# Optimization experiments

Hardware: AMD Instinct MI355X
Metric: run time of the kernel (lower is better)

Reference implementation:

```python
import jax, jax.numpy as jnp
import numpy as np

B, N, DIN, DOUT = 8, 2048, 512, 512

def setup_inputs() -> dict:
    key = jax.random.key(0)
    kx, ka, kw, kb, kattn = jax.random.split(key, 5)
    x = jax.random.normal(kx, (B, N, DIN), dtype=jnp.float32)
    adjacency_matrix = jax.random.randint(ka, (B, N, N), 0, 2, dtype=jnp.int32)
    # nn.Linear(in,out): weight [out,in], bias [out]
    lim_w = float(np.sqrt(1.0 / DIN))
    W = jax.random.uniform(kw, (DOUT, DIN), minval=-lim_w, maxval=lim_w, dtype=jnp.float32)
    b = jax.random.uniform(kb, (DOUT,), minval=-lim_w, maxval=lim_w, dtype=jnp.float32)
    # xavier_uniform for attn [out,out]
    lim_a = float(np.sqrt(6.0 / (DOUT + DOUT)))
    attn = jax.random.uniform(kattn, (DOUT, DOUT), minval=-lim_a, maxval=lim_a, dtype=jnp.float32)
    return {"x": x, "adjacency_matrix": adjacency_matrix, "W": W, "b": b, "attn": attn}

def reference(x, adjacency_matrix, W, b, attn):
    h = jnp.einsum('bni,oi->bno', x, W) + b                 # [B,N,DOUT]
    ha = jnp.einsum('bmi,ij->bmj', h, attn)                  # h @ attn
    scores = jnp.einsum('bmj,bnj->bmn', ha, h)               # bilinear pairwise scores
    scores = jnp.where(adjacency_matrix == 0, -jnp.inf, scores)
    attn_weights = jax.nn.softmax(scores, axis=-1)           # adjacency-masked softmax
    x_out = jnp.einsum('bmn,bnd->bmd', attn_weights, h)      # weighted aggregation
    return jax.nn.elu(x_out)
```

## Files before the change

kernel.cpp:

```cpp
#include <hip/hip_runtime.h>
#include <cstdint>
#include <cstddef>

typedef unsigned short u16;
using f16x8 = __attribute__((ext_vector_type(8))) _Float16;
using f32x4 = __attribute__((ext_vector_type(4))) float;
using u16x4 = __attribute__((ext_vector_type(4))) unsigned short;

__device__ __forceinline__ u16 f2h(float f) {
  union { _Float16 h; u16 u; } c;
  c.h = (_Float16)f;
  return c.u;
}

__device__ __forceinline__ void gl_lds16(const void* g, void* lds) {
  __builtin_amdgcn_global_load_lds(
      (const __attribute__((address_space(1))) void*)(uintptr_t)g,
      (__attribute__((address_space(3))) void*)(uint32_t)(uintptr_t)lds,
      16, 0, 0);
}

template <int MODE>
__global__ __launch_bounds__(256) void gemm_bt(
    const u16* __restrict__ A, const u16* __restrict__ Bt,
    void* __restrict__ Cv, const float* __restrict__ bias,
    int M, int Ncols, int K,
    long long strideA, long long strideB, long long strideC)
{
  __shared__ __align__(16) u16 sA[128 * 32];
  __shared__ __align__(16) u16 sB[128 * 32];

  const int bz = blockIdx.z;
  A  += (size_t)bz * strideA;
  Bt += (size_t)bz * strideB;

  const int m0 = blockIdx.y * 128;
  const int n0 = blockIdx.x * 128;
  const int t    = threadIdx.x;
  const int lane = t & 63;
  const int wave = t >> 6;
  const int wm   = (wave >> 1) * 64;
  const int wn   = (wave & 1) * 64;
  const int lm   = lane & 15;
  const int quad = lane >> 4;

  f32x4 acc[4][4];
#pragma unroll
  for (int i = 0; i < 4; ++i)
#pragma unroll
    for (int j = 0; j < 4; ++j) acc[i][j] = f32x4{0.f, 0.f, 0.f, 0.f};

  const int r0 = t >> 2,        c0 = t & 3;
  const int r1 = (t + 256) >> 2, c1 = t & 3;
  const int ldsb0 = (t & ~63) * 8;
  const int ldsb1 = ((t & ~63) + 256) * 8;

  const int nk = K >> 5;
  for (int kc = 0; kc < nk; ++kc) {
    const int kb = kc * 32;
    gl_lds16(A  + (size_t)(m0 + r0) * K + kb + c0 * 8, sA + ldsb0);
    gl_lds16(A  + (size_t)(m0 + r1) * K + kb + c1 * 8, sA + ldsb1);
    gl_lds16(Bt + (size_t)(n0 + r0) * K + kb + c0 * 8, sB + ldsb0);
    gl_lds16(Bt + (size_t)(n0 + r1) * K + kb + c1 * 8, sB + ldsb1);
    __syncthreads();

    f16x8 af[4], bf[4];
#pragma unroll
    for (int i = 0; i < 4; ++i) {
      af[i] = *(const f16x8*)(sA + (wm + i * 16 + lm) * 32 + quad * 8);
      bf[i] = *(const f16x8*)(sB + (wn + i * 16 + lm) * 32 + quad * 8);
    }
#pragma unroll
    for (int i = 0; i < 4; ++i)
#pragma unroll
      for (int j = 0; j < 4; ++j)
        acc[i][j] = __builtin_amdgcn_mfma_f32_16x16x32_f16(af[i], bf[j], acc[i][j], 0, 0, 0);
    __syncthreads();
  }

  u16* C = (u16*)Cv + (size_t)bz * strideC;
#pragma unroll
  for (int j = 0; j < 4; ++j) {
    const int col = n0 + wn + j * 16 + lm;
    const float bv = bias ? bias[col] : 0.f;
#pragma unroll
    for (int i = 0; i < 4; ++i)
#pragma unroll
      for (int r = 0; r < 4; ++r) {
        const int row = m0 + wm + i * 16 + quad * 4 + r;
        C[(size_t)row * Ncols + col] = f2h(acc[i][j][r] + bv);
      }
  }
}

__global__ __launch_bounds__(512, 2) void flash_gat(
    const u16* __restrict__ haP, const u16* __restrict__ hP,
    const u16* __restrict__ hTP, const u16* __restrict__ adjb,
    float* __restrict__ outP)
{
  __shared__ __align__(16) u16 sQ[2 * 64 * 32];
  __shared__ __align__(16) u16 sK[2 * 128 * 32];
  __shared__ __align__(16) u16 sP[64 * 136];
  __shared__ float rmA[4][64];
  __shared__ float rsA[4][64];
  __shared__ float m_sh[64], l_sh[64], al_sh[64];

  const int t     = threadIdx.x;
  const int batch = blockIdx.x & 7;
  const int q0    = (blockIdx.x >> 3) << 6;
  const int lane  = t & 63;
  const int wave  = t >> 6;
  const int lm    = lane & 15;
  const int quad  = lane >> 4;
  const int wm    = (wave >> 2) * 32;
  const int wn    = (wave & 3) * 32;
  const int wd    = wave * 64;

  const u16* Q  = haP + ((size_t)batch * 2048 + q0) * 512;
  const u16* K  = hP  + (size_t)batch * 2048 * 512;
  const u16* V  = hTP + (size_t)batch * 512 * 2048;
  const u16* Ar = adjb + ((size_t)batch * 2048 + q0) * 128;
  float* Co = outP + ((size_t)batch * 2048 + q0) * 512;

  if (t < 64) { m_sh[t] = -1e30f; l_sh[t] = 0.f; }

  f32x4 o[4][4];
#pragma unroll
  for (int i = 0; i < 4; ++i)
#pragma unroll
    for (int j = 0; j < 4; ++j) o[i][j] = f32x4{0.f, 0.f, 0.f, 0.f};

  const int kkq = t >> 8, rowq = (t >> 2) & 63, chq = t & 3;
  const u16* qsrc = Q + rowq * 512 + kkq * 32 + chq * 8;
  u16* qdst  = sQ + (t & ~63) * 8;
  const int rowk = t >> 2, chk = t & 3;
  u16* kdst0 = sK + (t & ~63) * 8;
  u16* kdst1 = sK + ((t & ~63) + 512) * 8;

  for (int nt = 0; nt < 16; ++nt) {
    const int n0 = nt * 128;
    f32x4 sacc[2][2];
#pragma unroll
    for (int i = 0; i < 2; ++i)
#pragma unroll
      for (int j = 0; j < 2; ++j) sacc[i][j] = f32x4{0.f, 0.f, 0.f, 0.f};

    const u16* Krow = K + (size_t)(n0 + rowk) * 512 + chk * 8;
    for (int kc = 0; kc < 8; ++kc) {
      const int kb = kc * 64;
      gl_lds16(qsrc + kb, qdst);
      gl_lds16(Krow + kb, kdst0);
      gl_lds16(Krow + kb + 32, kdst1);
      __syncthreads();
#pragma unroll
      for (int kk = 0; kk < 2; ++kk) {
        f16x8 aq[2], bk[2];
#pragma unroll
        for (int i = 0; i < 2; ++i)
          aq[i] = *(const f16x8*)(sQ + kk * 2048 + (wm + i * 16 + lm) * 32 + quad * 8);
#pragma unroll
        for (int j = 0; j < 2; ++j)
          bk[j] = *(const f16x8*)(sK + kk * 4096 + (wn + j * 16 + lm) * 32 + quad * 8);
#pragma unroll
        for (int i = 0; i < 2; ++i)
#pragma unroll
          for (int j = 0; j < 2; ++j)
            sacc[i][j] = __builtin_amdgcn_mfma_f32_16x16x32_f16(aq[i], bk[j], sacc[i][j], 0, 0, 0);
      }
      __syncthreads();
    }

#pragma unroll
    for (int i = 0; i < 2; ++i)
#pragma unroll
      for (int r = 0; r < 4; ++r) {
        const int R = wm + i * 16 + quad * 4 + r;
        const u16* ab = Ar + R * 128 + nt * 8 + (wn >> 4);
        const unsigned w0 = ab[0], w1 = ab[1];
        float s0 = sacc[i][0][r], s1 = sacc[i][1][r];
        s0 = ((w0 >> lm) & 1u) ? s0 : -1e30f;
        s1 = ((w1 >> lm) & 1u) ? s1 : -1e30f;
        sacc[i][0][r] = s0; sacc[i][1][r] = s1;
        float m = fmaxf(s0, s1);
        m = fmaxf(m, __shfl_xor(m, 1));
        m = fmaxf(m, __shfl_xor(m, 2));
        m = fmaxf(m, __shfl_xor(m, 4));
        m = fmaxf(m, __shfl_xor(m, 8));
        if (lm == 0) rmA[wave & 3][R] = m;
      }
    __syncthreads();

#pragma unroll
    for (int i = 0; i < 2; ++i)
#pragma unroll
      for (int r = 0; r < 4; ++r) {
        const int R = wm + i * 16 + quad * 4 + r;
        const float cm = fmaxf(fmaxf(rmA[0][R], rmA[1][R]), fmaxf(rmA[2][R], rmA[3][R]));
        const float nm = fmaxf(m_sh[R], cm);
        const float p0 = __expf(sacc[i][0][r] - nm);
        const float p1 = __expf(sacc[i][1][r] - nm);
        sP[R * 136 + wn + lm]      = f2h(p0);
        sP[R * 136 + wn + 16 + lm] = f2h(p1);
        float rr = p0 + p1;
        rr += __shfl_xor(rr, 1);
        rr += __shfl_xor(rr, 2);
        rr += __shfl_xor(rr, 4);
        rr += __shfl_xor(rr, 8);
        if (lm == 0) rsA[wave & 3][R] = rr;
      }
    __syncthreads();

    if (t < 64) {
      const float cm = fmaxf(fmaxf(rmA[0][t], rmA[1][t]), fmaxf(rmA[2][t], rmA[3][t]));
      const float mo = m_sh[t];
      const float nm = fmaxf(mo, cm);
      const float a  = __expf(mo - nm);
      l_sh[t]  = a * l_sh[t] + rsA[0][t] + rsA[1][t] + rsA[2][t] + rsA[3][t];
      m_sh[t]  = nm;
      al_sh[t] = a;
    }
    __syncthreads();

#pragma unroll
    for (int i = 0; i < 4; ++i)
#pragma unroll
      for (int r = 0; r < 4; ++r) {
        const float a = al_sh[i * 16 + quad * 4 + r];
#pragma unroll
        for (int j = 0; j < 4; ++j) o[i][j][r] *= a;
      }
#pragma unroll
    for (int kb = 0; kb < 4; ++kb) {
      f16x8 ap[4], bv[4];
#pragma unroll
      for (int i = 0; i < 4; ++i)
        ap[i] = *(const f16x8*)(sP + (i * 16 + lm) * 136 + kb * 32 + quad * 8);
#pragma unroll
      for (int j = 0; j < 4; ++j)
        bv[j] = *(const f16x8*)(V + (size_t)(wd + j * 16 + lm) * 2048 + n0 + kb * 32 + quad * 8);
#pragma unroll
      for (int i = 0; i < 4; ++i)
#pragma unroll
        for (int j = 0; j < 4; ++j)
          o[i][j] = __builtin_amdgcn_mfma_f32_16x16x32_f16(ap[i], bv[j], o[i][j], 0, 0, 0);
    }
  }

#pragma unroll
  for (int i = 0; i < 4; ++i)
#pragma unroll
    for (int r = 0; r < 4; ++r) {
      const int R = i * 16 + quad * 4 + r;
      const float inv = 1.f / l_sh[R];
#pragma unroll
      for (int j = 0; j < 4; ++j) {
        float v = o[i][j][r] * inv;
        v = v > 0.f ? v : expm1f(v);
        Co[(size_t)R * 512 + wd + j * 16 + lm] = v;
      }
    }
}

__global__ __launch_bounds__(256) void adj_pack(
    const int* __restrict__ adj, u16* __restrict__ outw, int nwords)
{
  const int i = blockIdx.x * 256 + threadIdx.x;
  if (i >= nwords) return;
  const int4* p = (const int4*)(adj + (size_t)i * 16);
  unsigned w = 0;
#pragma unroll
  for (int k = 0; k < 4; ++k) {
    int4 v = p[k];
    w |= (unsigned)(v.x != 0) << (k * 4 + 0);
    w |= (unsigned)(v.y != 0) << (k * 4 + 1);
    w |= (unsigned)(v.z != 0) << (k * 4 + 2);
    w |= (unsigned)(v.w != 0) << (k * 4 + 3);
  }
  outw[i] = (u16)w;
}

__global__ __launch_bounds__(256) void transpose_u16(
    const u16* __restrict__ in, u16* __restrict__ outp, int R, int C)
{
  __shared__ u16 tile[64][65];
  const size_t base = (size_t)blockIdx.z * R * C;
  const int r0 = blockIdx.y * 64, c0 = blockIdx.x * 64;
  const int t = threadIdx.x;
  const int c = t & 63, rr = t >> 6;
#pragma unroll
  for (int i = 0; i < 16; ++i) {
    const int r = rr + i * 4;
    tile[r][c] = in[base + (size_t)(r0 + r) * C + c0 + c];
  }
  __syncthreads();
  const int rp = t & 63, cc = t >> 6;
#pragma unroll
  for (int i = 0; i < 16; ++i) {
    const int cq = cc + i * 4;
    outp[base + (size_t)(c0 + cq) * R + r0 + rp] = tile[rp][cq];
  }
}

__global__ __launch_bounds__(256) void cvt_f32_f16(
    const float* __restrict__ in, u16* __restrict__ outp, int n4)
{
  const int i = blockIdx.x * 256 + threadIdx.x;
  if (i >= n4) return;
  float4 v = ((const float4*)in)[i];
  u16x4 o; o[0] = f2h(v.x); o[1] = f2h(v.y); o[2] = f2h(v.z); o[3] = f2h(v.w);
  ((u16x4*)outp)[i] = o;
}

__global__ __launch_bounds__(256) void transpose_cvt(
    const float* __restrict__ in, u16* __restrict__ outp, int R, int C)
{
  const int idx = blockIdx.x * 256 + threadIdx.x;
  const int i = idx / C, j = idx % C;
  outp[(size_t)j * R + i] = f2h(in[idx]);
}

extern "C" void kernel_launch(void* const* d_in, const int* in_sizes, int n_in,
                              void* d_out, int out_size, void* d_ws, size_t ws_size,
                              hipStream_t stream) {
  (void)in_sizes; (void)n_in; (void)out_size;
  const float* x    = (const float*)d_in[0];
  const int*   adj  = (const int*)d_in[1];
  const float* W    = (const float*)d_in[2];
  const float* bvec = (const float*)d_in[3];
  const float* attn = (const float*)d_in[4];
  float* out = (float*)d_out;

  constexpr int B = 8, N = 2048, D = 512;
  constexpr size_t MN = (size_t)B * N;

  char* ws = (char*)d_ws;
  size_t off = 0;
  auto take = [&](size_t bytes) -> char* {
    char* p = ws + off;
    off += (bytes + 255) & ~(size_t)255;
    return p;
  };
  u16* xh   = (u16*)take(MN * D * 2);
  u16* Wh   = (u16*)take((size_t)D * D * 2);
  u16* attT = (u16*)take((size_t)D * D * 2);
  u16* h    = (u16*)take(MN * D * 2);
  u16* hT   = (u16*)take(MN * D * 2);
  u16* ha   = (u16*)take(MN * D * 2);
  u16* adjb = (u16*)take((size_t)B * N * (N / 16) * 2);
  if (off > ws_size) return;

  cvt_f32_f16<<<dim3((unsigned)(MN * D / 4 / 256)), 256, 0, stream>>>(x, xh, (int)(MN * D / 4));
  cvt_f32_f16<<<dim3(D * D / 4 / 256), 256, 0, stream>>>(W, Wh, D * D / 4);
  transpose_cvt<<<dim3(D * D / 256), 256, 0, stream>>>(attn, attT, D, D);
  const int nwords = (int)(MN * (N / 16));
  adj_pack<<<dim3(nwords / 256), 256, 0, stream>>>(adj, adjb, nwords);

  gemm_bt<0><<<dim3(D / 128, MN / 128, 1), 256, 0, stream>>>(
      xh, Wh, h, bvec, (int)MN, D, D, 0, 0, 0);
  transpose_u16<<<dim3(D / 64, N / 64, B), 256, 0, stream>>>(h, hT, N, D);
  gemm_bt<0><<<dim3(D / 128, MN / 128, 1), 256, 0, stream>>>(
      h, attT, ha, nullptr, (int)MN, D, D, 0, 0, 0);

  flash_gat<<<dim3(256), 512, 0, stream>>>(ha, h, hT, adjb, out);
}
```

Before: 508.7 us.

## Fuse h transpose into GEMM epilogue and retile flash kernel to 32-row blocks

```diff
diff --git a/kernel.cpp b/kernel.cpp
--- a/kernel.cpp
+++ b/kernel.cpp
@@ -23,16 +23,11 @@
 template <int MODE>
 __global__ __launch_bounds__(256) void gemm_bt(
     const u16* __restrict__ A, const u16* __restrict__ Bt,
-    void* __restrict__ Cv, const float* __restrict__ bias,
-    int M, int Ncols, int K,
-    long long strideA, long long strideB, long long strideC)
+    u16* __restrict__ C, const float* __restrict__ bias,
+    u16* __restrict__ hTp, int Ncols, int K)
 {
   __shared__ __align__(16) u16 sA[128 * 32];
   __shared__ __align__(16) u16 sB[128 * 32];
-
-  const int bz = blockIdx.z;
-  A  += (size_t)bz * strideA;
-  Bt += (size_t)bz * strideB;
 
   const int m0 = blockIdx.y * 128;
   const int n0 = blockIdx.x * 128;
@@ -50,8 +45,8 @@
 #pragma unroll
     for (int j = 0; j < 4; ++j) acc[i][j] = f32x4{0.f, 0.f, 0.f, 0.f};
 
-  const int r0 = t >> 2,        c0 = t & 3;
-  const int r1 = (t + 256) >> 2, c1 = t & 3;
+  const int r0 = t >> 2,         c0 = t & 3;
+  const int r1 = (t + 256) >> 2;
   const int ldsb0 = (t & ~63) * 8;
   const int ldsb1 = ((t & ~63) + 256) * 8;
 
@@ -59,9 +54,9 @@
   for (int kc = 0; kc < nk; ++kc) {
     const int kb = kc * 32;
     gl_lds16(A  + (size_t)(m0 + r0) * K + kb + c0 * 8, sA + ldsb0);
-    gl_lds16(A  + (size_t)(m0 + r1) * K + kb + c1 * 8, sA + ldsb1);
+    gl_lds16(A  + (size_t)(m0 + r1) * K + kb + c0 * 8, sA + ldsb1);
     gl_lds16(Bt + (size_t)(n0 + r0) * K + kb + c0 * 8, sB + ldsb0);
-    gl_lds16(Bt + (size_t)(n0 + r1) * K + kb + c1 * 8, sB + ldsb1);
+    gl_lds16(Bt + (size_t)(n0 + r1) * K + kb + c0 * 8, sB + ldsb1);
     __syncthreads();
 
     f16x8 af[4], bf[4];
@@ -78,43 +73,49 @@
     __syncthreads();
   }
 
-  u16* C = (u16*)Cv + (size_t)bz * strideC;
 #pragma unroll
   for (int j = 0; j < 4; ++j) {
     const int col = n0 + wn + j * 16 + lm;
     const float bv = bias ? bias[col] : 0.f;
 #pragma unroll
-    for (int i = 0; i < 4; ++i)
+    for (int i = 0; i < 4; ++i) {
+      const int row0 = m0 + wm + i * 16 + quad * 4;
+      u16x4 tp;
 #pragma unroll
       for (int r = 0; r < 4; ++r) {
-        const int row = m0 + wm + i * 16 + quad * 4 + r;
-        C[(size_t)row * Ncols + col] = f2h(acc[i][j][r] + bv);
-      }
+        const u16 hv = f2h(acc[i][j][r] + bv);
+        C[(size_t)(row0 + r) * Ncols + col] = hv;
+        tp[r] = hv;
+      }
+      if (MODE == 3) {
+        const int b = row0 >> 11, n = row0 & 2047;
+        *(u16x4*)(hTp + ((size_t)b * 512 + col) * 2048 + n) = tp;
+      }
+    }
   }
 }
 
-__global__ __launch_bounds__(512, 2) void flash_gat(
+__global__ __launch_bounds__(256, 2) void flash_gat(
     const u16* __restrict__ haP, const u16* __restrict__ hP,
     const u16* __restrict__ hTP, const u16* __restrict__ adjb,
     float* __restrict__ outP)
 {
-  __shared__ __align__(16) u16 sQ[2 * 64 * 32];
-  __shared__ __align__(16) u16 sK[2 * 128 * 32];
-  __shared__ __align__(16) u16 sP[64 * 136];
-  __shared__ float rmA[4][64];
-  __shared__ float rsA[4][64];
-  __shared__ float m_sh[64], l_sh[64], al_sh[64];
+  __shared__ __align__(16) u16 sQ[4 * 32 * 32];
+  __shared__ __align__(16) u16 sK[4 * 128 * 32];
+  __shared__ __align__(16) u16 sP[32 * 136];
+  __shared__ float rmA[2][32], rsA[2][32];
+  __shared__ float m_sh[32], l_sh[32], al_sh[32];
 
   const int t     = threadIdx.x;
   const int batch = blockIdx.x & 7;
-  const int q0    = (blockIdx.x >> 3) << 6;
+  const int q0    = (blockIdx.x >> 3) << 5;
   const int lane  = t & 63;
   const int wave  = t >> 6;
   const int lm    = lane & 15;
   const int quad  = lane >> 4;
-  const int wm    = (wave >> 2) * 32;
-  const int wn    = (wave & 3) * 32;
-  const int wd    = wave * 64;
+  const int wqm   = (wave >> 1) * 16;
+  const int wqn   = (wave & 1) * 64;
+  const int wd    = wave * 128;
 
   const u16* Q  = haP + ((size_t)batch * 2048 + q0) * 512;
   const u16* K  = hP  + (size_t)batch * 2048 * 512;
@@ -122,138 +123,135 @@
   const u16* Ar = adjb + ((size_t)batch * 2048 + q0) * 128;
   float* Co = outP + ((size_t)batch * 2048 + q0) * 512;
 
-  if (t < 64) { m_sh[t] = -1e30f; l_sh[t] = 0.f; }
-
-  f32x4 o[4][4];
-#pragma unroll
-  for (int i = 0; i < 4; ++i)
-#pragma unroll
-    for (int j = 0; j < 4; ++j) o[i][j] = f32x4{0.f, 0.f, 0.f, 0.f};
-
-  const int kkq = t >> 8, rowq = (t >> 2) & 63, chq = t & 3;
-  const u16* qsrc = Q + rowq * 512 + kkq * 32 + chq * 8;
-  u16* qdst  = sQ + (t & ~63) * 8;
-  const int rowk = t >> 2, chk = t & 3;
-  u16* kdst0 = sK + (t & ~63) * 8;
-  u16* kdst1 = sK + ((t & ~63) + 512) * 8;
+  if (t < 32) { m_sh[t] = -1e30f; l_sh[t] = 0.f; }
+
+  f32x4 o[2][8];
+#pragma unroll
+  for (int i = 0; i < 2; ++i)
+#pragma unroll
+    for (int j = 0; j < 8; ++j) o[i][j] = f32x4{0.f, 0.f, 0.f, 0.f};
 
   for (int nt = 0; nt < 16; ++nt) {
     const int n0 = nt * 128;
-    f32x4 sacc[2][2];
-#pragma unroll
-    for (int i = 0; i < 2; ++i)
-#pragma unroll
-      for (int j = 0; j < 2; ++j) sacc[i][j] = f32x4{0.f, 0.f, 0.f, 0.f};
-
-    const u16* Krow = K + (size_t)(n0 + rowk) * 512 + chk * 8;
-    for (int kc = 0; kc < 8; ++kc) {
-      const int kb = kc * 64;
-      gl_lds16(qsrc + kb, qdst);
-      gl_lds16(Krow + kb, kdst0);
-      gl_lds16(Krow + kb + 32, kdst1);
+    f32x4 sacc[4];
+#pragma unroll
+    for (int j = 0; j < 4; ++j) sacc[j] = f32x4{0.f, 0.f, 0.f, 0.f};
+
+    for (int kc = 0; kc < 4; ++kc) {
+#pragma unroll
+      for (int c = 0; c < 8; ++c) {
+        const int s = c * 256 + t;
+        const int q = s & 3, r = (s >> 2) & 127, pk = s >> 9;
+        gl_lds16(K + (size_t)(n0 + r) * 512 + kc * 128 + pk * 32 + q * 8,
+                 sK + (size_t)(c * 256 + (t & ~63)) * 8);
+      }
+#pragma unroll
+      for (int c = 0; c < 2; ++c) {
+        const int s = c * 256 + t;
+        const int q = s & 3, r = (s >> 2) & 31, p = s >> 7;
+        gl_lds16(Q + (size_t)r * 512 + kc * 128 + p * 32 + q * 8,
+                 sQ + (size_t)(c * 256 + (t & ~63)) * 8);
+      }
       __syncthreads();
-#pragma unroll
-      for (int kk = 0; kk < 2; ++kk) {
-        f16x8 aq[2], bk[2];
-#pragma unroll
-        for (int i = 0; i < 2; ++i)
-          aq[i] = *(const f16x8*)(sQ + kk * 2048 + (wm + i * 16 + lm) * 32 + quad * 8);
-#pragma unroll
-        for (int j = 0; j < 2; ++j)
-          bk[j] = *(const f16x8*)(sK + kk * 4096 + (wn + j * 16 + lm) * 32 + quad * 8);
-#pragma unroll
-        for (int i = 0; i < 2; ++i)
-#pragma unroll
-          for (int j = 0; j < 2; ++j)
-            sacc[i][j] = __builtin_amdgcn_mfma_f32_16x16x32_f16(aq[i], bk[j], sacc[i][j], 0, 0, 0);
+
+#pragma unroll
+      for (int kk = 0; kk < 4; ++kk) {
+        const f16x8 aq = *(const f16x8*)(sQ + kk * 1024 + (wqm + lm) * 32 + quad * 8);
+        f16x8 bk[4];
+#pragma unroll
+        for (int j = 0; j < 4; ++j)
+          bk[j] = *(const f16x8*)(sK + kk * 4096 + (wqn + j * 16 + lm) * 32 + quad * 8);
+#pragma unroll
+        for (int j = 0; j < 4; ++j)
+          sacc[j] = __builtin_amdgcn_mfma_f32_16x16x32_f16(aq, bk[j], sacc[j], 0, 0, 0);
       }
       __syncthreads();
     }
 
 #pragma unroll
-    for (int i = 0; i < 2; ++i)
-#pragma unroll
-      for (int r = 0; r < 4; ++r) {
-        const int R = wm + i * 16 + quad * 4 + r;
-        const u16* ab = Ar + R * 128 + nt * 8 + (wn >> 4);
-        const unsigned w0 = ab[0], w1 = ab[1];
-        float s0 = sacc[i][0][r], s1 = sacc[i][1][r];
-        s0 = ((w0 >> lm) & 1u) ? s0 : -1e30f;
-        s1 = ((w1 >> lm) & 1u) ? s1 : -1e30f;
-        sacc[i][0][r] = s0; sacc[i][1][r] = s1;
-        float m = fmaxf(s0, s1);
-        m = fmaxf(m, __shfl_xor(m, 1));
-        m = fmaxf(m, __shfl_xor(m, 2));
-        m = fmaxf(m, __shfl_xor(m, 4));
-        m = fmaxf(m, __shfl_xor(m, 8));
-        if (lm == 0) rmA[wave & 3][R] = m;
-      }
-    __syncthreads();
-
-#pragma unroll
-    for (int i = 0; i < 2; ++i)
-#pragma unroll
-      for (int r = 0; r < 4; ++r) {
-        const int R = wm + i * 16 + quad * 4 + r;
-        const float cm = fmaxf(fmaxf(rmA[0][R], rmA[1][R]), fmaxf(rmA[2][R], rmA[3][R]));
-        const float nm = fmaxf(m_sh[R], cm);
-        const float p0 = __expf(sacc[i][0][r] - nm);
-        const float p1 = __expf(sacc[i][1][r] - nm);
-        sP[R * 136 + wn + lm]      = f2h(p0);
-        sP[R * 136 + wn + 16 + lm] = f2h(p1);
-        float rr = p0 + p1;
-        rr += __shfl_xor(rr, 1);
-        rr += __shfl_xor(rr, 2);
-        rr += __shfl_xor(rr, 4);
-        rr += __shfl_xor(rr, 8);
-        if (lm == 0) rsA[wave & 3][R] = rr;
-      }
-    __syncthreads();
-
-    if (t < 64) {
-      const float cm = fmaxf(fmaxf(rmA[0][t], rmA[1][t]), fmaxf(rmA[2][t], rmA[3][t]));
+    for (int r = 0; r < 4; ++r) {
+      const int R = wqm + quad * 4 + r;
+      const u16x4 aw = *(const u16x4*)(Ar + (size_t)R * 128 + nt * 8 + (wqn >> 4));
+      float mx = -1e30f;
+#pragma unroll
+      for (int j = 0; j < 4; ++j) {
+        float s = sacc[j][r];
+        s = ((aw[j] >> lm) & 1u) ? s : -1e30f;
+        sacc[j][r] = s;
+        mx = fmaxf(mx, s);
+      }
+      mx = fmaxf(mx, __shfl_xor(mx, 1));
+      mx = fmaxf(mx, __shfl_xor(mx, 2));
+      mx = fmaxf(mx, __shfl_xor(mx, 4));
+      mx = fmaxf(mx, __shfl_xor(mx, 8));
+      if (lm == 0) rmA[wave & 1][R] = mx;
+    }
+    __syncthreads();
+
+#pragma unroll
+    for (int r = 0; r < 4; ++r) {
+      const int R = wqm + quad * 4 + r;
+      const float cm = fmaxf(rmA[0][R], rmA[1][R]);
+      const float nm = fmaxf(m_sh[R], cm);
+      float rs = 0.f;
+#pragma unroll
+      for (int j = 0; j < 4; ++j) {
+        const float p = __expf(sacc[j][r] - nm);
+        rs += p;
+        sP[R * 136 + wqn + j * 16 + lm] = f2h(p);
+      }
+      rs += __shfl_xor(rs, 1);
+      rs += __shfl_xor(rs, 2);
+      rs += __shfl_xor(rs, 4);
+      rs += __shfl_xor(rs, 8);
+      if (lm == 0) rsA[wave & 1][R] = rs;
+    }
+    __syncthreads();
+
+    if (t < 32) {
+      const float cm = fmaxf(rmA[0][t], rmA[1][t]);
       const float mo = m_sh[t];
       const float nm = fmaxf(mo, cm);
       const float a  = __expf(mo - nm);
-      l_sh[t]  = a * l_sh[t] + rsA[0][t] + rsA[1][t] + rsA[2][t] + rsA[3][t];
+      l_sh[t]  = a * l_sh[t] + rsA[0][t] + rsA[1][t];
       m_sh[t]  = nm;
       al_sh[t] = a;
     }
     __syncthreads();
 
 #pragma unroll
-    for (int i = 0; i < 4; ++i)
+    for (int i = 0; i < 2; ++i)
 #pragma unroll
       for (int r = 0; r < 4; ++r) {
         const float a = al_sh[i * 16 + quad * 4 + r];
 #pragma unroll
-        for (int j = 0; j < 4; ++j) o[i][j][r] *= a;
+        for (int j = 0; j < 8; ++j) o[i][j][r] *= a;
       }
 #pragma unroll
     for (int kb = 0; kb < 4; ++kb) {
-      f16x8 ap[4], bv[4];
-#pragma unroll
-      for (int i = 0; i < 4; ++i)
+      f16x8 ap[2], bv[8];
+#pragma unroll
+      for (int i = 0; i < 2; ++i)
         ap[i] = *(const f16x8*)(sP + (i * 16 + lm) * 136 + kb * 32 + quad * 8);
 #pragma unroll
-      for (int j = 0; j < 4; ++j)
+      for (int j = 0; j < 8; ++j)
         bv[j] = *(const f16x8*)(V + (size_t)(wd + j * 16 + lm) * 2048 + n0 + kb * 32 + quad * 8);
 #pragma unroll
-      for (int i = 0; i < 4; ++i)
-#pragma unroll
-        for (int j = 0; j < 4; ++j)
+      for (int i = 0; i < 2; ++i)
+#pragma unroll
+        for (int j = 0; j < 8; ++j)
           o[i][j] = __builtin_amdgcn_mfma_f32_16x16x32_f16(ap[i], bv[j], o[i][j], 0, 0, 0);
     }
   }
 
 #pragma unroll
-  for (int i = 0; i < 4; ++i)
+  for (int i = 0; i < 2; ++i)
 #pragma unroll
     for (int r = 0; r < 4; ++r) {
       const int R = i * 16 + quad * 4 + r;
       const float inv = 1.f / l_sh[R];
 #pragma unroll
-      for (int j = 0; j < 4; ++j) {
+      for (int j = 0; j < 8; ++j) {
         float v = o[i][j][r] * inv;
         v = v > 0.f ? v : expm1f(v);
         Co[(size_t)R * 512 + wd + j * 16 + lm] = v;
@@ -277,28 +275,6 @@
     w |= (unsigned)(v.w != 0) << (k * 4 + 3);
   }
   outw[i] = (u16)w;
-}
-
-__global__ __launch_bounds__(256) void transpose_u16(
-    const u16* __restrict__ in, u16* __restrict__ outp, int R, int C)
-{
-  __shared__ u16 tile[64][65];
-  const size_t base = (size_t)blockIdx.z * R * C;
-  const int r0 = blockIdx.y * 64, c0 = blockIdx.x * 64;
-  const int t = threadIdx.x;
-  const int c = t & 63, rr = t >> 6;
-#pragma unroll
-  for (int i = 0; i < 16; ++i) {
-    const int r = rr + i * 4;
-    tile[r][c] = in[base + (size_t)(r0 + r) * C + c0 + c];
-  }
-  __syncthreads();
-  const int rp = t & 63, cc = t >> 6;
-#pragma unroll
-  for (int i = 0; i < 16; ++i) {
-    const int cq = cc + i * 4;
-    outp[base + (size_t)(c0 + cq) * R + r0 + rp] = tile[rp][cq];
-  }
 }
 
 __global__ __launch_bounds__(256) void cvt_f32_f16(
@@ -355,11 +331,10 @@
   const int nwords = (int)(MN * (N / 16));
   adj_pack<<<dim3(nwords / 256), 256, 0, stream>>>(adj, adjb, nwords);
 
-  gemm_bt<0><<<dim3(D / 128, MN / 128, 1), 256, 0, stream>>>(
-      xh, Wh, h, bvec, (int)MN, D, D, 0, 0, 0);
-  transpose_u16<<<dim3(D / 64, N / 64, B), 256, 0, stream>>>(h, hT, N, D);
-  gemm_bt<0><<<dim3(D / 128, MN / 128, 1), 256, 0, stream>>>(
-      h, attT, ha, nullptr, (int)MN, D, D, 0, 0, 0);
-
-  flash_gat<<<dim3(256), 512, 0, stream>>>(ha, h, hT, adjb, out);
-}
+  gemm_bt<3><<<dim3(D / 128, MN / 128), 256, 0, stream>>>(
+      xh, Wh, h, bvec, hT, D, D);
+  gemm_bt<0><<<dim3(D / 128, MN / 128), 256, 0, stream>>>(
+      h, attT, ha, nullptr, nullptr, D, D);
+
+  flash_gat<<<dim3(512), 256, 0, stream>>>(ha, h, hT, adjb, out);
+}
```

After: 496.1 us. 2.5% less time.
